# Kernel optimization log

Hardware: AMD Instinct MI355X
Metric: run time of the kernel (lower is better)

The kernel has to match this reference:

```python
import jax, jax.numpy as jnp
import numpy as np

K = 1024
D = 128


def setup_inputs() -> dict:
    key = jax.random.key(0)
    ks = jax.random.split(key, 6)
    span_repr = jax.random.normal(ks[0], (K, D), dtype=jnp.float32)
    antecedents_repr = jax.random.normal(ks[1], (K, D), dtype=jnp.float32)
    # PyTorch Linear init scale ~ 1/sqrt(fan_in)
    W1 = jax.random.normal(ks[2], (3 * D, D), dtype=jnp.float32) / np.sqrt(3 * D)
    b1 = jax.random.normal(ks[3], (D,), dtype=jnp.float32) / np.sqrt(3 * D)
    W2 = jax.random.normal(ks[4], (D, 1), dtype=jnp.float32) / np.sqrt(D)
    b2 = jax.random.normal(ks[5], (1,), dtype=jnp.float32) / np.sqrt(D)
    return {"span_repr": span_repr, "antecedents_repr": antecedents_repr,
            "W1": W1, "b1": b1, "W2": W2, "b2": b2}


def reference(span_repr, antecedents_repr, W1, b1, W2, b2):
    k = span_repr.shape[0]
    # strictly-lower-triangular pairs (i > j), same order as the nested loops
    i_idx, j_idx = jnp.tril_indices(k, -1)  # row-major over i, then j < i
    si = span_repr[i_idx]            # [P, D]
    aj = antecedents_repr[j_idx]     # [P, D]
    feats = jnp.concatenate([si, aj, si - aj], axis=-1)  # [P, 3D]
    h = jax.nn.relu(feats @ W1 + b1)                     # [P, D]
    scores = (h @ W2 + b2)[:, 0]                         # [P]
    out = jnp.zeros((k, k), dtype=span_repr.dtype).at[i_idx, j_idx].set(scores)
    return out
```

## Files before the change

kernel.cpp:

```cpp
#include <hip/hip_runtime.h>

#define KDIM 1024
#define DDIM 128
#define TS   32
#define LDP  132

__global__ __launch_bounds__(256) void prep_uv(
    const float* __restrict__ span, const float* __restrict__ ant,
    const float* __restrict__ W1,   const float* __restrict__ b1,
    float* __restrict__ U, float* __restrict__ V)
{
    __shared__ float a_lds[16 * DDIM];

    const int mat  = blockIdx.x & 1;
    const int rblk = blockIdx.x >> 1;
    const float* __restrict__ A = mat ? ant : span;
    float* __restrict__ outp    = mat ? V : U;
    const int tid = threadIdx.x;

    {
        const float4* src = (const float4*)(A + rblk * 16 * DDIM);
        float4* dst = (float4*)a_lds;
        dst[tid]       = src[tid];
        dst[tid + 256] = src[tid + 256];
    }
    __syncthreads();

    const int c  = tid & 127;
    const int rg = tid >> 7;
    float acc[8];
    const float binit = mat ? 0.0f : b1[c];
#pragma unroll
    for (int r = 0; r < 8; ++r) acc[r] = binit;

    const float* __restrict__ Wx = W1 + (mat ? DDIM * DDIM : 0);
    const float* __restrict__ Wc = W1 + 2 * DDIM * DDIM;
    const float sgn = mat ? -1.0f : 1.0f;

    for (int d0 = 0; d0 < DDIM; d0 += 4) {
        float w[4];
#pragma unroll
        for (int dd = 0; dd < 4; ++dd)
            w[dd] = Wx[(d0 + dd) * DDIM + c] + sgn * Wc[(d0 + dd) * DDIM + c];
#pragma unroll
        for (int r = 0; r < 8; ++r) {
            float4 a4 = *(const float4*)&a_lds[(rg * 8 + r) * DDIM + d0];
            acc[r] += a4.x * w[0] + a4.y * w[1] + a4.z * w[2] + a4.w * w[3];
        }
    }

#pragma unroll
    for (int r = 0; r < 8; ++r)
        outp[(rblk * 16 + rg * 8 + r) * DDIM + c] = acc[r];
}

__global__ __launch_bounds__(256) void pair_score(
    const float* __restrict__ U, const float* __restrict__ V,
    const float* __restrict__ W2, const float* __restrict__ b2,
    float* __restrict__ out)
{
    const int bj = blockIdx.x;
    const int bi = blockIdx.y;
    const int tid = threadIdx.x;

    if (bi < bj) {
        const int r  = tid >> 3;
        const int c4 = (tid & 7) << 2;
        *(float4*)&out[(bi * TS + r) * KDIM + bj * TS + c4] =
            make_float4(0.f, 0.f, 0.f, 0.f);
        return;
    }

    __shared__ float Ul[TS * LDP];
    __shared__ float Vl[TS * LDP];
    __shared__ float W2l[DDIM];

    {
        const float4* us = (const float4*)(U + bi * TS * DDIM);
        const float4* vs = (const float4*)(V + bj * TS * DDIM);
#pragma unroll
        for (int k = 0; k < 4; ++k) {
            int idx = tid + k * 256;
            int r   = idx >> 5;
            int c4  = idx & 31;
            *(float4*)&Ul[r * LDP + c4 * 4] = us[idx];
            *(float4*)&Vl[r * LDP + c4 * 4] = vs[idx];
        }
        if (tid < 32) *(float4*)&W2l[tid * 4] = *(const float4*)&W2[tid * 4];
    }
    __syncthreads();

    const int tj = tid & 15;
    const int ti = tid >> 4;
    const int i0 = ti * 2;
    const int j0 = tj * 2;
    const float b2v = b2[0];
    float a00 = b2v, a01 = b2v, a10 = b2v, a11 = b2v;

#pragma unroll
    for (int d = 0; d < DDIM; d += 4) {
        float4 u0 = *(const float4*)&Ul[i0 * LDP + d];
        float4 u1 = *(const float4*)&Ul[(i0 + 1) * LDP + d];
        float4 v0 = *(const float4*)&Vl[j0 * LDP + d];
        float4 v1 = *(const float4*)&Vl[(j0 + 1) * LDP + d];
        float4 w  = *(const float4*)&W2l[d];
#define STEP(C)                                   \
        a00 += fmaxf(u0.C + v0.C, 0.f) * w.C;     \
        a01 += fmaxf(u0.C + v1.C, 0.f) * w.C;     \
        a10 += fmaxf(u1.C + v0.C, 0.f) * w.C;     \
        a11 += fmaxf(u1.C + v1.C, 0.f) * w.C;
        STEP(x) STEP(y) STEP(z) STEP(w)
#undef STEP
    }

    const int gi0 = bi * TS + i0;
    const int gj0 = bj * TS + j0;
    float2 r0, r1;
    r0.x = (gi0     > gj0    ) ? a00 : 0.f;
    r0.y = (gi0     > gj0 + 1) ? a01 : 0.f;
    r1.x = (gi0 + 1 > gj0    ) ? a10 : 0.f;
    r1.y = (gi0 + 1 > gj0 + 1) ? a11 : 0.f;
    *(float2*)&out[ gi0      * KDIM + gj0] = r0;
    *(float2*)&out[(gi0 + 1) * KDIM + gj0] = r1;
}

extern "C" void kernel_launch(void* const* d_in, const int* in_sizes, int n_in,
                              void* d_out, int out_size, void* d_ws, size_t ws_size,
                              hipStream_t stream)
{
    const float* span = (const float*)d_in[0];
    const float* ant  = (const float*)d_in[1];
    const float* W1   = (const float*)d_in[2];
    const float* b1   = (const float*)d_in[3];
    const float* W2   = (const float*)d_in[4];
    const float* b2   = (const float*)d_in[5];
    float* out = (float*)d_out;

    float* U = (float*)d_ws;
    float* V = U + KDIM * DDIM;

    prep_uv<<<dim3(128), 256, 0, stream>>>(span, ant, W1, b1, U, V);
    pair_score<<<dim3(32, 32), 256, 0, stream>>>(U, V, W2, b2, out);
}
```

Measured before the change: 24.21 us.

## Use 4x4 register tiles with packed float2 math in pair_score, shrink prep blocks

Each pair_score block now runs 64 threads instead of 256, and each thread computes a 4x4 strided tile of pair scores rather than 2x2. The inner loop uses two-wide float vectors for add, max and multiply, aiming at packed FP32 instructions and more register reuse per LDS load. prep_uv moves to 8-row blocks with twice as many blocks to fill more CUs. The trade-off is fewer waves per block and higher register pressure, which may cut occupancy, while the strided stores are less coalesced.

```diff
diff --git a/kernel.cpp b/kernel.cpp
--- a/kernel.cpp
+++ b/kernel.cpp
@@ -2,15 +2,16 @@
 
 #define KDIM 1024
 #define DDIM 128
-#define TS   32
 #define LDP  132
+
+typedef float f2 __attribute__((ext_vector_type(2)));
 
 __global__ __launch_bounds__(256) void prep_uv(
     const float* __restrict__ span, const float* __restrict__ ant,
     const float* __restrict__ W1,   const float* __restrict__ b1,
     float* __restrict__ U, float* __restrict__ V)
 {
-    __shared__ float a_lds[16 * DDIM];
+    __shared__ float a_lds[8 * DDIM];
 
     const int mat  = blockIdx.x & 1;
     const int rblk = blockIdx.x >> 1;
@@ -19,19 +20,17 @@
     const int tid = threadIdx.x;
 
     {
-        const float4* src = (const float4*)(A + rblk * 16 * DDIM);
-        float4* dst = (float4*)a_lds;
-        dst[tid]       = src[tid];
-        dst[tid + 256] = src[tid + 256];
+        const float4* src = (const float4*)(A + rblk * 8 * DDIM);
+        ((float4*)a_lds)[tid] = src[tid];
     }
     __syncthreads();
 
     const int c  = tid & 127;
     const int rg = tid >> 7;
-    float acc[8];
+    float acc[4];
     const float binit = mat ? 0.0f : b1[c];
 #pragma unroll
-    for (int r = 0; r < 8; ++r) acc[r] = binit;
+    for (int r = 0; r < 4; ++r) acc[r] = binit;
 
     const float* __restrict__ Wx = W1 + (mat ? DDIM * DDIM : 0);
     const float* __restrict__ Wc = W1 + 2 * DDIM * DDIM;
@@ -43,44 +42,48 @@
         for (int dd = 0; dd < 4; ++dd)
             w[dd] = Wx[(d0 + dd) * DDIM + c] + sgn * Wc[(d0 + dd) * DDIM + c];
 #pragma unroll
-        for (int r = 0; r < 8; ++r) {
-            float4 a4 = *(const float4*)&a_lds[(rg * 8 + r) * DDIM + d0];
+        for (int r = 0; r < 4; ++r) {
+            float4 a4 = *(const float4*)&a_lds[(rg * 4 + r) * DDIM + d0];
             acc[r] += a4.x * w[0] + a4.y * w[1] + a4.z * w[2] + a4.w * w[3];
         }
     }
 
 #pragma unroll
-    for (int r = 0; r < 8; ++r)
-        outp[(rblk * 16 + rg * 8 + r) * DDIM + c] = acc[r];
+    for (int r = 0; r < 4; ++r)
+        outp[(rblk * 8 + rg * 4 + r) * DDIM + c] = acc[r];
 }
 
-__global__ __launch_bounds__(256) void pair_score(
+__global__ __launch_bounds__(64) void pair_score(
     const float* __restrict__ U, const float* __restrict__ V,
     const float* __restrict__ W2, const float* __restrict__ b2,
     float* __restrict__ out)
 {
-    const int bj = blockIdx.x;
-    const int bi = blockIdx.y;
+    const int bj  = blockIdx.x;
+    const int bi  = blockIdx.y;
     const int tid = threadIdx.x;
 
     if (bi < bj) {
-        const int r  = tid >> 3;
-        const int c4 = (tid & 7) << 2;
-        *(float4*)&out[(bi * TS + r) * KDIM + bj * TS + c4] =
-            make_float4(0.f, 0.f, 0.f, 0.f);
+        const float4 z4 = make_float4(0.f, 0.f, 0.f, 0.f);
+#pragma unroll
+        for (int k = 0; k < 8; ++k) {
+            int idx = tid + k * 64;
+            int r   = idx >> 3;
+            int c4  = idx & 7;
+            *(float4*)&out[(bi * 32 + r) * KDIM + bj * 32 + c4 * 4] = z4;
+        }
         return;
     }
 
-    __shared__ float Ul[TS * LDP];
-    __shared__ float Vl[TS * LDP];
+    __shared__ float Ul[32 * LDP];
+    __shared__ float Vl[32 * LDP];
     __shared__ float W2l[DDIM];
 
     {
-        const float4* us = (const float4*)(U + bi * TS * DDIM);
-        const float4* vs = (const float4*)(V + bj * TS * DDIM);
+        const float4* us = (const float4*)(U + bi * 32 * DDIM);
+        const float4* vs = (const float4*)(V + bj * 32 * DDIM);
 #pragma unroll
-        for (int k = 0; k < 4; ++k) {
-            int idx = tid + k * 256;
+        for (int k = 0; k < 16; ++k) {
+            int idx = tid + k * 64;
             int r   = idx >> 5;
             int c4  = idx & 31;
             *(float4*)&Ul[r * LDP + c4 * 4] = us[idx];
@@ -90,38 +93,58 @@
     }
     __syncthreads();
 
-    const int tj = tid & 15;
-    const int ti = tid >> 4;
-    const int i0 = ti * 2;
-    const int j0 = tj * 2;
-    const float b2v = b2[0];
-    float a00 = b2v, a01 = b2v, a10 = b2v, a11 = b2v;
+    const int tj = tid & 7;
+    const int ti = tid >> 3;
+    const f2 z2 = {0.f, 0.f};
 
+    f2 acc[4][4][2];
 #pragma unroll
+    for (int a = 0; a < 4; ++a)
+#pragma unroll
+        for (int b = 0; b < 4; ++b) {
+            acc[a][b][0] = z2; acc[a][b][1] = z2;
+        }
+
+#pragma unroll 4
     for (int d = 0; d < DDIM; d += 4) {
-        float4 u0 = *(const float4*)&Ul[i0 * LDP + d];
-        float4 u1 = *(const float4*)&Ul[(i0 + 1) * LDP + d];
-        float4 v0 = *(const float4*)&Vl[j0 * LDP + d];
-        float4 v1 = *(const float4*)&Vl[(j0 + 1) * LDP + d];
-        float4 w  = *(const float4*)&W2l[d];
-#define STEP(C)                                   \
-        a00 += fmaxf(u0.C + v0.C, 0.f) * w.C;     \
-        a01 += fmaxf(u0.C + v1.C, 0.f) * w.C;     \
-        a10 += fmaxf(u1.C + v0.C, 0.f) * w.C;     \
-        a11 += fmaxf(u1.C + v1.C, 0.f) * w.C;
-        STEP(x) STEP(y) STEP(z) STEP(w)
-#undef STEP
+        f2 ul[4][2], vl[4][2], w[2];
+        {
+            float4 x = *(const float4*)&W2l[d];
+            w[0] = f2{x.x, x.y}; w[1] = f2{x.z, x.w};
+        }
+#pragma unroll
+        for (int a = 0; a < 4; ++a) {
+            float4 x = *(const float4*)&Ul[(ti + 8 * a) * LDP + d];
+            ul[a][0] = f2{x.x, x.y}; ul[a][1] = f2{x.z, x.w};
+        }
+#pragma unroll
+        for (int b = 0; b < 4; ++b) {
+            float4 x = *(const float4*)&Vl[(tj + 8 * b) * LDP + d];
+            vl[b][0] = f2{x.x, x.y}; vl[b][1] = f2{x.z, x.w};
+        }
+#pragma unroll
+        for (int a = 0; a < 4; ++a)
+#pragma unroll
+            for (int b = 0; b < 4; ++b) {
+                f2 t0 = __builtin_elementwise_max(ul[a][0] + vl[b][0], z2);
+                f2 t1 = __builtin_elementwise_max(ul[a][1] + vl[b][1], z2);
+                acc[a][b][0] += t0 * w[0];
+                acc[a][b][1] += t1 * w[1];
+            }
     }
 
-    const int gi0 = bi * TS + i0;
-    const int gj0 = bj * TS + j0;
-    float2 r0, r1;
-    r0.x = (gi0     > gj0    ) ? a00 : 0.f;
-    r0.y = (gi0     > gj0 + 1) ? a01 : 0.f;
-    r1.x = (gi0 + 1 > gj0    ) ? a10 : 0.f;
-    r1.y = (gi0 + 1 > gj0 + 1) ? a11 : 0.f;
-    *(float2*)&out[ gi0      * KDIM + gj0] = r0;
-    *(float2*)&out[(gi0 + 1) * KDIM + gj0] = r1;
+    const float b2v = b2[0];
+#pragma unroll
+    for (int a = 0; a < 4; ++a) {
+        const int gi = bi * 32 + ti + 8 * a;
+#pragma unroll
+        for (int b = 0; b < 4; ++b) {
+            const int gj = bj * 32 + tj + 8 * b;
+            f2 s2 = acc[a][b][0] + acc[a][b][1];
+            float s = s2.x + s2.y + b2v;
+            out[gi * KDIM + gj] = (gi > gj) ? s : 0.f;
+        }
+    }
 }
 
 extern "C" void kernel_launch(void* const* d_in, const int* in_sizes, int n_in,
@@ -139,6 +162,6 @@
     float* U = (float*)d_ws;
     float* V = U + KDIM * DDIM;
 
-    prep_uv<<<dim3(128), 256, 0, stream>>>(span, ant, W1, b1, U, V);
-    pair_score<<<dim3(32, 32), 256, 0, stream>>>(U, V, W2, b2, out);
+    prep_uv<<<dim3(256), 256, 0, stream>>>(span, ant, W1, b1, U, V);
+    pair_score<<<dim3(32, 32), 64, 0, stream>>>(U, V, W2, b2, out);
 }
```

After: 23.62 us. -2.4%, faster.
